# Optimization experiments

Measured on AMD Instinct MI355X. Metric: run time of the kernel, lower is better.

## Reference

```python
import jax, jax.numpy as jnp
import numpy as np

N = 100000       # nodes
E = 3200000      # edges (avg degree 32)
NFEAT = 500
NHID = 256
NCLASS = 40
NLAYERS = 5
EPS = 1e-5


def layer_norm(x, g, b):
    mu = jnp.mean(x, axis=-1, keepdims=True)
    var = jnp.mean(jnp.square(x - mu), axis=-1, keepdims=True)
    return (x - mu) * jax.lax.rsqrt(var + EPS) * g + b


def spmm(row, col, val, x):
    # out[i] = sum_{e: row[e]==i} val[e] * x[col[e]]  == adj @ x
    return jax.ops.segment_sum(val[:, None] * x[col], row, num_segments=N)


def setup_inputs() -> dict:
    key = jax.random.key(0)
    ks = jax.random.split(key, 10)
    s_in = 1.0 / np.sqrt(NFEAT)
    s_h = 1.0 / np.sqrt(NHID)
    return {
        "x": jax.random.normal(ks[0], (N, NFEAT), jnp.float32),
        "row": jax.random.randint(ks[1], (E,), 0, N, jnp.int32),
        "col": jax.random.randint(ks[2], (E,), 0, N, jnp.int32),
        "val": jax.random.uniform(ks[3], (E,), jnp.float32) * (1.0 / 32.0),
        "in_W": jax.random.normal(ks[4], (NHID, NFEAT), jnp.float32) * s_in,
        "in_b": jnp.zeros((NHID,), jnp.float32),
        "convW": jax.random.normal(ks[5], (NLAYERS, NHID, NHID), jnp.float32) * s_h,
        "convB": jnp.zeros((NLAYERS, NHID), jnp.float32),
        "lnG": jnp.ones((NLAYERS, NHID), jnp.float32),
        "lnB": jnp.zeros((NLAYERS, NHID), jnp.float32),
        "outG": jnp.ones((NHID,), jnp.float32),
        "outB": jnp.zeros((NHID,), jnp.float32),
        "out_W": jax.random.normal(ks[6], (NCLASS, NHID), jnp.float32) * s_h,
        "out_b": jnp.zeros((NCLASS,), jnp.float32),
        "only_z": 1,
    }


def reference(x, row, col, val, in_W, in_b, convW, convB, lnG, lnB,
              outG, outB, out_W, out_b, only_z):
    # input layer (input_dropout=0, so dropout is identity)
    h = jax.nn.relu(x @ in_W.T + in_b)
    # residual GCN layers with pre-LayerNorm (norm['flag'] == True)
    for i in range(NLAYERS):
        r = layer_norm(h, lnG[i], lnB[i])
        r = spmm(row, col, val, r)          # sparse aggregation
        r = r @ convW[i].T + convB[i]       # single linear (n_linear=1)
        if i < NLAYERS - 1:                 # last conv has last_layer=True -> no act
            r = jax.nn.relu(r)
        h = h + r
    mid = h                                 # captured at i == n_layers-1 (post-residual)
    z = layer_norm(h, outG, outB) @ out_W.T + out_b  # squeeze(1) is a no-op for nclass=40
    if only_z:
        return z
    return (mid, z)
```

## Files before the change

### kernel.cpp

```cpp
#include <hip/hip_runtime.h>
#include <stdint.h>

#define NFEAT 500
#define KPAD  512
#define NHID  256
#define NCLS  40
#define NCPAD 48
#define NLAY  5
#define BSH   8
#define CHUNK 8192

typedef __attribute__((ext_vector_type(8))) short short8;
typedef __attribute__((ext_vector_type(4))) float f32x4;

__device__ __forceinline__ ushort f2bf(float f) {
  uint32_t u = __float_as_uint(f);
  u += 0x7fffu + ((u >> 16) & 1u);
  return (ushort)(u >> 16);
}
__device__ __forceinline__ float b2f(ushort h) {
  return __uint_as_float(((uint32_t)h) << 16);
}

__global__ __launch_bounds__(256) void k_cast_pad(const float* __restrict__ src,
    ushort* __restrict__ dst, int rows, int scol, int dcol) {
  int id = blockIdx.x * 256 + threadIdx.x;
  int cpr = dcol >> 2;
  if (id >= rows * cpr) return;
  int r = id / cpr;
  int c = (id % cpr) * 4;
  float4 v;
  if (c + 3 < scol) {
    v = *(const float4*)(src + (size_t)r * scol + c);
  } else {
    v.x = (c + 0 < scol) ? src[(size_t)r * scol + c + 0] : 0.f;
    v.y = (c + 1 < scol) ? src[(size_t)r * scol + c + 1] : 0.f;
    v.z = (c + 2 < scol) ? src[(size_t)r * scol + c + 2] : 0.f;
    v.w = (c + 3 < scol) ? src[(size_t)r * scol + c + 3] : 0.f;
  }
  ushort4 o;
  o.x = f2bf(v.x); o.y = f2bf(v.y); o.z = f2bf(v.z); o.w = f2bf(v.w);
  *(ushort4*)(dst + (size_t)r * dcol + c) = o;
}

__global__ __launch_bounds__(256) void kA_scatter(const int* __restrict__ row,
    const int* __restrict__ col, const float* __restrict__ val,
    int* __restrict__ ccur, int2* __restrict__ pb, int E, int P, int CAP) {
  __shared__ int lh[512];
  const int t = threadIdx.x;
  const int b0 = blockIdx.x * CHUNK;
  for (int i = t; i < P; i += 256) lh[i] = 0;
  __syncthreads();
#pragma unroll 4
  for (int i = 0; i < CHUNK / 256; i++) {
    int idx = b0 + i * 256 + t;
    if (idx < E) atomicAdd(&lh[row[idx] >> BSH], 1);
  }
  __syncthreads();
  for (int i = t; i < P; i += 256) {
    int c = lh[i];
    lh[i] = (c > 0) ? atomicAdd(&ccur[i], c) : 0;
  }
  __syncthreads();
#pragma unroll 4
  for (int i = 0; i < CHUNK / 256; i++) {
    int idx = b0 + i * 256 + t;
    if (idx < E) {
      int r = row[idx];
      int p = r >> BSH;
      int pos = atomicAdd(&lh[p], 1);
      if (pos < CAP)
        pb[(size_t)p * CAP + pos] =
            make_int2(col[idx] | ((r & 255) << 24), __float_as_int(val[idx]));
    }
  }
}

__global__ __launch_bounds__(256) void kB_cnt(const int* __restrict__ ccur,
    const int2* __restrict__ pb, int* __restrict__ cnt, int* __restrict__ bsum,
    int N, int CAP) {
  __shared__ int lc[256];
  __shared__ int ws[4];
  const int b = blockIdx.x;
  const int t = threadIdx.x;
  lc[t] = 0;
  __syncthreads();
  int cb = min(ccur[b], CAP);
  size_t base = (size_t)b * CAP;
  for (int i = t; i < cb; i += 256)
    atomicAdd(&lc[((uint32_t)pb[base + i].x) >> 24], 1);
  __syncthreads();
  int c = lc[t];
  int r = (b << BSH) + t;
  if (r < N) cnt[r] = c;
  int v = c;
  v += __shfl_xor(v, 1); v += __shfl_xor(v, 2); v += __shfl_xor(v, 4);
  v += __shfl_xor(v, 8); v += __shfl_xor(v, 16); v += __shfl_xor(v, 32);
  if ((t & 63) == 0) ws[t >> 6] = v;
  __syncthreads();
  if (t == 0) bsum[b] = ws[0] + ws[1] + ws[2] + ws[3];
}

__global__ __launch_bounds__(1024) void k_scanP(const int* __restrict__ bsum,
    int* __restrict__ boff, int* __restrict__ ptrN, int P) {
  __shared__ int ls[1024];
  int t = threadIdx.x;
  int v = (t < P) ? bsum[t] : 0;
  ls[t] = v;
  __syncthreads();
  for (int off = 1; off < 1024; off <<= 1) {
    int u = (t >= off) ? ls[t - off] : 0;
    __syncthreads();
    ls[t] += u;
    __syncthreads();
  }
  if (t < P) boff[t] = ls[t] - v;
  if (t == 1023) *ptrN = ls[1023];
}

__global__ __launch_bounds__(256) void kB_ptr(const int* __restrict__ cnt,
    const int* __restrict__ boff, int* __restrict__ ptr, int N) {
  __shared__ int ls[256];
  int b = blockIdx.x;
  int t = threadIdx.x;
  int r = (b << BSH) + t;
  int v = (r < N) ? cnt[r] : 0;
  ls[t] = v;
  __syncthreads();
  for (int off = 1; off < 256; off <<= 1) {
    int u = (t >= off) ? ls[t - off] : 0;
    __syncthreads();
    ls[t] += u;
    __syncthreads();
  }
  if (r < N) ptr[r] = boff[b] + ls[t] - v;
}

__global__ __launch_bounds__(256) void kB_scatter(const int* __restrict__ ccur,
    const int2* __restrict__ pb, const int* __restrict__ ptr,
    int2* __restrict__ cv, int CAP) {
  __shared__ int rk[256];
  const int b = blockIdx.x;
  rk[threadIdx.x] = 0;
  __syncthreads();
  int cb = min(ccur[b], CAP);
  size_t base = (size_t)b * CAP;
  for (int i = threadIdx.x; i < cb; i += 256) {
    int2 p2 = pb[base + i];
    int r8 = ((uint32_t)p2.x) >> 24;
    int r = (b << BSH) + r8;
    int rank = atomicAdd(&rk[r8], 1);
    cv[ptr[r] + rank] = make_int2(p2.x & 0x00FFFFFF, p2.y);
  }
}

template<int FP8OUT>
__global__ __launch_bounds__(256) void k_ln(const float* __restrict__ h,
    const float* __restrict__ g, const float* __restrict__ b,
    void* __restrict__ o, int n) {
  int r = (blockIdx.x * 256 + threadIdx.x) >> 6;
  int lane = threadIdx.x & 63;
  if (r >= n) return;
  float4 v = *(const float4*)(h + (size_t)r * NHID + lane * 4);
  float s = v.x + v.y + v.z + v.w;
  s += __shfl_xor(s, 1); s += __shfl_xor(s, 2); s += __shfl_xor(s, 4);
  s += __shfl_xor(s, 8); s += __shfl_xor(s, 16); s += __shfl_xor(s, 32);
  float mu = s * (1.f / NHID);
  float d0 = v.x - mu, d1 = v.y - mu, d2 = v.z - mu, d3 = v.w - mu;
  float q = d0 * d0 + d1 * d1 + d2 * d2 + d3 * d3;
  q += __shfl_xor(q, 1); q += __shfl_xor(q, 2); q += __shfl_xor(q, 4);
  q += __shfl_xor(q, 8); q += __shfl_xor(q, 16); q += __shfl_xor(q, 32);
  float rs = rsqrtf(q * (1.f / NHID) + 1e-5f);
  float4 gv = *(const float4*)(g + lane * 4);
  float4 bv = *(const float4*)(b + lane * 4);
  float o0 = d0 * rs * gv.x + bv.x;
  float o1 = d1 * rs * gv.y + bv.y;
  float o2 = d2 * rs * gv.z + bv.z;
  float o3 = d3 * rs * gv.w + bv.w;
  if (FP8OUT) {
    int w = 0;
    w = __builtin_amdgcn_cvt_pk_fp8_f32(o0, o1, w, false);
    w = __builtin_amdgcn_cvt_pk_fp8_f32(o2, o3, w, true);
    ((uint32_t*)o)[(size_t)r * 64 + lane] = (uint32_t)w;
  } else {
    ushort4 t;
    t.x = f2bf(o0); t.y = f2bf(o1); t.z = f2bf(o2); t.w = f2bf(o3);
    *(ushort4*)((ushort*)o + (size_t)r * NHID + lane * 4) = t;
  }
}

__global__ __launch_bounds__(256) void k_spmm(const int* __restrict__ ptr,
    const int2* __restrict__ cv, const uint32_t* __restrict__ t8,
    ushort* __restrict__ agg, int n) {
  int r = (blockIdx.x * 256 + threadIdx.x) >> 6;
  int lane = threadIdx.x & 63;
  if (r >= n) return;
  int s = ptr[r], e = ptr[r + 1];
  int cnt = e - s;
  int half = lane >> 5;
  int seg = lane & 31;
  float acc[8];
#pragma unroll
  for (int j = 0; j < 8; j++) acc[j] = 0.f;

  for (int base = 0; base < cnt; base += 64) {
    int idx = s + base + lane;
    int ec = 0; float ev = 0.f;
    if (idx < e) {
      int2 p2 = cv[idx];
      ec = p2.x;
      ev = __uint_as_float((uint32_t)p2.y);
    }
    int lim = min(64, cnt - base);
#pragma unroll 2
    for (int i = 0; i < lim; i += 2) {
      int a = i + half;
      int c = __shfl(ec, a);
      float v = __shfl(ev, a);
      uint2 tv = *(const uint2*)(t8 + (size_t)c * 64 + seg * 2);
      auto p0 = __builtin_amdgcn_cvt_pk_f32_fp8(tv.x, false);
      auto p1 = __builtin_amdgcn_cvt_pk_f32_fp8(tv.x, true);
      auto p2 = __builtin_amdgcn_cvt_pk_f32_fp8(tv.y, false);
      auto p3 = __builtin_amdgcn_cvt_pk_f32_fp8(tv.y, true);
      acc[0] += v * p0[0]; acc[1] += v * p0[1];
      acc[2] += v * p1[0]; acc[3] += v * p1[1];
      acc[4] += v * p2[0]; acc[5] += v * p2[1];
      acc[6] += v * p3[0]; acc[7] += v * p3[1];
    }
  }

#pragma unroll
  for (int j = 0; j < 8; j++) acc[j] += __shfl_xor(acc[j], 32);
  if (half == 0) {
    short8 o;
#pragma unroll
    for (int j = 0; j < 8; j++) o[j] = (short)f2bf(acc[j]);
    *(short8*)(agg + (size_t)r * NHID + seg * 8) = o;
  }
}

template<int MODE>
__global__ __launch_bounds__(256) void k_gemm(const ushort* __restrict__ A,
    const ushort* __restrict__ B, const float* __restrict__ bias,
    float* __restrict__ H, int M, int K) {
  __shared__ ushort As[128 * 32];
  __shared__ ushort Bs[128 * 32];
  const int t = threadIdx.x;
  const int lane = t & 63;
  const int wid = t >> 6;
  const int brow = blockIdx.x * 128;
  const int bcol = blockIdx.y * 128;
  const int wr = (wid >> 1) * 64;
  const int wc = (wid & 1) * 64;
  const int l15 = lane & 15, hi = lane >> 4;
  const f32x4 z4 = {0.f, 0.f, 0.f, 0.f};
  f32x4 acc[4][4];
  for (int m = 0; m < 4; m++)
    for (int n = 0; n < 4; n++) acc[m][n] = z4;

  for (int k0 = 0; k0 < K; k0 += 32) {
    __syncthreads();
#pragma unroll
    for (int c = 0; c < 2; c++) {
      int s = c * 256 + t;
      int r = s >> 2;
      int kk = (s & 3) * 8;
      int gr = brow + r; gr = gr < M ? gr : M - 1;
      const ushort* ga = A + (size_t)gr * K + (k0 + kk);
      __builtin_amdgcn_global_load_lds((const __attribute__((address_space(1))) void*)ga,
          (__attribute__((address_space(3))) void*)(As + s * 8), 16, 0, 0);
      const ushort* gb = B + (size_t)(bcol + r) * K + (k0 + kk);
      __builtin_amdgcn_global_load_lds((const __attribute__((address_space(1))) void*)gb,
          (__attribute__((address_space(3))) void*)(Bs + s * 8), 16, 0, 0);
    }
    __syncthreads();
    short8 af[4], bf[4];
#pragma unroll
    for (int m = 0; m < 4; m++)
      af[m] = *(const short8*)(As + (wr + m * 16 + l15) * 32 + hi * 8);
#pragma unroll
    for (int n = 0; n < 4; n++)
      bf[n] = *(const short8*)(Bs + (wc + n * 16 + l15) * 32 + hi * 8);
#pragma unroll
    for (int m = 0; m < 4; m++)
#pragma unroll
      for (int n = 0; n < 4; n++)
        acc[m][n] = __builtin_amdgcn_mfma_f32_16x16x32_bf16(af[m], bf[n], acc[m][n], 0, 0, 0);
  }

#pragma unroll
  for (int m = 0; m < 4; m++) {
    int gr0 = brow + wr + m * 16 + hi * 4;
#pragma unroll
    for (int n = 0; n < 4; n++) {
      int gc = bcol + wc + n * 16 + l15;
      float bv = bias[gc];
#pragma unroll
      for (int j = 0; j < 4; j++) {
        int gr = gr0 + j;
        if (gr < M) {
          size_t idx = (size_t)gr * NHID + gc;
          float v = acc[m][n][j] + bv;
          if (MODE == 0)      H[idx] = fmaxf(v, 0.f);
          else if (MODE == 1) H[idx] += fmaxf(v, 0.f);
          else                H[idx] += v;
        }
      }
    }
  }
}

__global__ __launch_bounds__(256) void k_ogemm(const ushort* __restrict__ A,
    const ushort* __restrict__ Bw, const float* __restrict__ ob,
    float* __restrict__ z, int M) {
  __shared__ ushort As[256 * 32];
  __shared__ ushort Bs[NCPAD * 264];
  const int t = threadIdx.x;
  const int lane = t & 63;
  const int wid = t >> 6;
  const int brow = blockIdx.x * 256;
  const int wr = wid * 64;
  const int l15 = lane & 15, hi = lane >> 4;
  const f32x4 z4 = {0.f, 0.f, 0.f, 0.f};
  f32x4 acc[4][3];
#pragma unroll
  for (int m = 0; m < 4; m++)
#pragma unroll
    for (int n = 0; n < 3; n++) acc[m][n] = z4;

  for (int i = t; i < NCPAD * 33; i += 256) {
    int r = i / 33, cc = i % 33;
    if (cc < 32)
      *(short8*)(Bs + r * 264 + cc * 8) = *(const short8*)(Bw + r * 256 + cc * 8);
  }

  for (int k0 = 0; k0 < 256; k0 += 32) {
    __syncthreads();
#pragma unroll
    for (int c = 0; c < 4; c++) {
      int s = c * 256 + t;
      int r = s >> 2;
      int kk = (s & 3) * 8;
      int gr = brow + r; gr = gr < M ? gr : M - 1;
      const ushort* ga = A + (size_t)gr * NHID + (k0 + kk);
      __builtin_amdgcn_global_load_lds((const __attribute__((address_space(1))) void*)ga,
          (__attribute__((address_space(3))) void*)(As + s * 8), 16, 0, 0);
    }
    __syncthreads();
    short8 af[4], bf[3];
#pragma unroll
    for (int m = 0; m < 4; m++)
      af[m] = *(const short8*)(As + (wr + m * 16 + l15) * 32 + hi * 8);
#pragma unroll
    for (int n = 0; n < 3; n++)
      bf[n] = *(const short8*)(Bs + (n * 16 + l15) * 264 + k0 + hi * 8);
#pragma unroll
    for (int m = 0; m < 4; m++)
#pragma unroll
      for (int n = 0; n < 3; n++)
        acc[m][n] = __builtin_amdgcn_mfma_f32_16x16x32_bf16(af[m], bf[n], acc[m][n], 0, 0, 0);
  }

#pragma unroll
  for (int m = 0; m < 4; m++) {
    int gr0 = brow + wr + m * 16 + hi * 4;
#pragma unroll
    for (int n = 0; n < 3; n++) {
      int gc = n * 16 + l15;
      if (gc < NCLS) {
        float bv = ob[gc];
#pragma unroll
        for (int j = 0; j < 4; j++) {
          int gr = gr0 + j;
          if (gr < M) z[(size_t)gr * NCLS + gc] = acc[m][n][j] + bv;
        }
      }
    }
  }
}

extern "C" void kernel_launch(void* const* d_in, const int* in_sizes, int n_in,
                              void* d_out, int out_size, void* d_ws, size_t ws_size,
                              hipStream_t stream) {
  const float* x     = (const float*)d_in[0];
  const int*   row   = (const int*)d_in[1];
  const int*   col   = (const int*)d_in[2];
  const float* val   = (const float*)d_in[3];
  const float* inW   = (const float*)d_in[4];
  const float* inB   = (const float*)d_in[5];
  const float* convW = (const float*)d_in[6];
  const float* convB = (const float*)d_in[7];
  const float* lnG   = (const float*)d_in[8];
  const float* lnB   = (const float*)d_in[9];
  const float* outG  = (const float*)d_in[10];
  const float* outB  = (const float*)d_in[11];
  const float* outW  = (const float*)d_in[12];
  const float* outb  = (const float*)d_in[13];
  const int N = in_sizes[0] / NFEAT;
  const int E = in_sizes[1];
  float* z = (float*)d_out;

  const int P   = (N + 255) >> BSH;
  const int CAP = ((((E + P - 1) / P) * 5 / 4 + 256) + 15) & ~15;

  char* wsp = (char*)d_ws;
  size_t off = 0;
  auto alloc = [&](size_t bytes) {
    void* p = wsp + off;
    off += (bytes + 255) & ~(size_t)255;
    return p;
  };
  float*    h   = (float*)alloc((size_t)N * NHID * 4);
  ushort*   tb  = (ushort*)alloc((size_t)N * NHID * 2);
  ushort*   ab  = (ushort*)alloc((size_t)N * NHID * 2);
  uint32_t* t8  = (uint32_t*)alloc((size_t)N * 64 * 4);
  ushort*   xb  = (ushort*)alloc((size_t)N * KPAD * 2);
  ushort*   wbi = (ushort*)alloc((size_t)NHID * KPAD * 2);
  ushort*   wbc = (ushort*)alloc((size_t)NLAY * NHID * NHID * 2);
  ushort*   wbo = (ushort*)alloc((size_t)NCPAD * NHID * 2);
  int*   cnt  = (int*)alloc((size_t)N * 4);
  int*   ptr  = (int*)alloc((size_t)(N + 1) * 4);
  int*   ccur = (int*)alloc((size_t)P * 4);
  int*   bsum = (int*)alloc((size_t)P * 4);
  int*   boff = (int*)alloc((size_t)P * 4);
  int2*  cv   = (int2*)alloc((size_t)E * 8);
  int2*  pb   = (int2*)xb;

  {
    int tot = N * (KPAD >> 2);
    k_cast_pad<<<(tot + 255) / 256, 256, 0, stream>>>(x, xb, N, NFEAT, KPAD);
    tot = NHID * (KPAD >> 2);
    k_cast_pad<<<(tot + 255) / 256, 256, 0, stream>>>(inW, wbi, NHID, NFEAT, KPAD);
    tot = NLAY * NHID * (NHID >> 2);
    k_cast_pad<<<(tot + 255) / 256, 256, 0, stream>>>(convW, wbc, NLAY * NHID, NHID, NHID);
    hipMemsetAsync(wbo, 0, (size_t)NCPAD * NHID * 2, stream);
    tot = NCLS * (NHID >> 2);
    k_cast_pad<<<(tot + 255) / 256, 256, 0, stream>>>(outW, wbo, NCLS, NHID, NHID);
  }

  dim3 gg((N + 127) / 128, NHID / 128);
  k_gemm<0><<<gg, 256, 0, stream>>>(xb, wbi, inB, h, N, KPAD);

  hipMemsetAsync(ccur, 0, (size_t)P * 4, stream);
  kA_scatter<<<(E + CHUNK - 1) / CHUNK, 256, 0, stream>>>(row, col, val, ccur, pb, E, P, CAP);
  kB_cnt<<<P, 256, 0, stream>>>(ccur, pb, cnt, bsum, N, CAP);
  k_scanP<<<1, 1024, 0, stream>>>(bsum, boff, ptr + N, P);
  kB_ptr<<<P, 256, 0, stream>>>(cnt, boff, ptr, N);
  kB_scatter<<<P, 256, 0, stream>>>(ccur, pb, ptr, cv, CAP);

  int nwb = (N + 3) / 4;
  for (int i = 0; i < NLAY; i++) {
    k_ln<1><<<nwb, 256, 0, stream>>>(h, lnG + i * NHID, lnB + i * NHID, t8, N);
    k_spmm<<<nwb, 256, 0, stream>>>(ptr, cv, t8, ab, N);
    if (i < NLAY - 1)
      k_gemm<1><<<gg, 256, 0, stream>>>(ab, wbc + (size_t)i * NHID * NHID,
                                        convB + i * NHID, h, N, NHID);
    else
      k_gemm<2><<<gg, 256, 0, stream>>>(ab, wbc + (size_t)i * NHID * NHID,
                                        convB + i * NHID, h, N, NHID);
  }

  k_ln<0><<<nwb, 256, 0, stream>>>(h, outG, outB, tb, N);
  k_ogemm<<<(N + 255) / 256, 256, 0, stream>>>(tb, wbo, outb, z, N);
}
```

Measured before the change: 1.421 ms.

## Store residual hidden state in bf16 and widen SpMM per-lane gathers

The residual stream h changes from fp32 to bf16, which halves the read-modify-write traffic in the GEMM epilogues and the reads in the LayerNorm kernels. Separately, the SpMM kernel now has each lane load 16 fp8 values (uint4) and processes four edges per wave iteration instead of two, then reduces across quarter-waves. Accumulating the residual in bf16 through five layers lowers precision. The SpMM change also raises register use per thread and leaves fewer lanes writing output.

```diff
diff --git a/kernel.cpp b/kernel.cpp
--- a/kernel.cpp
+++ b/kernel.cpp
@@ -155,18 +155,19 @@
 }
 
 template<int FP8OUT>
-__global__ __launch_bounds__(256) void k_ln(const float* __restrict__ h,
+__global__ __launch_bounds__(256) void k_ln(const ushort* __restrict__ h,
     const float* __restrict__ g, const float* __restrict__ b,
     void* __restrict__ o, int n) {
   int r = (blockIdx.x * 256 + threadIdx.x) >> 6;
   int lane = threadIdx.x & 63;
   if (r >= n) return;
-  float4 v = *(const float4*)(h + (size_t)r * NHID + lane * 4);
-  float s = v.x + v.y + v.z + v.w;
+  ushort4 hv = *(const ushort4*)(h + (size_t)r * NHID + lane * 4);
+  float v0 = b2f(hv.x), v1 = b2f(hv.y), v2 = b2f(hv.z), v3 = b2f(hv.w);
+  float s = v0 + v1 + v2 + v3;
   s += __shfl_xor(s, 1); s += __shfl_xor(s, 2); s += __shfl_xor(s, 4);
   s += __shfl_xor(s, 8); s += __shfl_xor(s, 16); s += __shfl_xor(s, 32);
   float mu = s * (1.f / NHID);
-  float d0 = v.x - mu, d1 = v.y - mu, d2 = v.z - mu, d3 = v.w - mu;
+  float d0 = v0 - mu, d1 = v1 - mu, d2 = v2 - mu, d3 = v3 - mu;
   float q = d0 * d0 + d1 * d1 + d2 * d2 + d3 * d3;
   q += __shfl_xor(q, 1); q += __shfl_xor(q, 2); q += __shfl_xor(q, 4);
   q += __shfl_xor(q, 8); q += __shfl_xor(q, 16); q += __shfl_xor(q, 32);
@@ -197,11 +198,11 @@
   if (r >= n) return;
   int s = ptr[r], e = ptr[r + 1];
   int cnt = e - s;
-  int half = lane >> 5;
-  int seg = lane & 31;
-  float acc[8];
-#pragma unroll
-  for (int j = 0; j < 8; j++) acc[j] = 0.f;
+  int q = lane >> 4;
+  int seg = lane & 15;
+  float acc[16];
+#pragma unroll
+  for (int j = 0; j < 16; j++) acc[j] = 0.f;
 
   for (int base = 0; base < cnt; base += 64) {
     int idx = s + base + lane;
@@ -213,36 +214,48 @@
     }
     int lim = min(64, cnt - base);
 #pragma unroll 2
-    for (int i = 0; i < lim; i += 2) {
-      int a = i + half;
+    for (int i = 0; i < lim; i += 4) {
+      int a = i + q;
       int c = __shfl(ec, a);
       float v = __shfl(ev, a);
-      uint2 tv = *(const uint2*)(t8 + (size_t)c * 64 + seg * 2);
+      uint4 tv = *(const uint4*)(t8 + (size_t)c * 64 + seg * 4);
       auto p0 = __builtin_amdgcn_cvt_pk_f32_fp8(tv.x, false);
       auto p1 = __builtin_amdgcn_cvt_pk_f32_fp8(tv.x, true);
       auto p2 = __builtin_amdgcn_cvt_pk_f32_fp8(tv.y, false);
       auto p3 = __builtin_amdgcn_cvt_pk_f32_fp8(tv.y, true);
-      acc[0] += v * p0[0]; acc[1] += v * p0[1];
-      acc[2] += v * p1[0]; acc[3] += v * p1[1];
-      acc[4] += v * p2[0]; acc[5] += v * p2[1];
-      acc[6] += v * p3[0]; acc[7] += v * p3[1];
-    }
-  }
-
-#pragma unroll
-  for (int j = 0; j < 8; j++) acc[j] += __shfl_xor(acc[j], 32);
-  if (half == 0) {
-    short8 o;
-#pragma unroll
-    for (int j = 0; j < 8; j++) o[j] = (short)f2bf(acc[j]);
-    *(short8*)(agg + (size_t)r * NHID + seg * 8) = o;
+      auto p4 = __builtin_amdgcn_cvt_pk_f32_fp8(tv.z, false);
+      auto p5 = __builtin_amdgcn_cvt_pk_f32_fp8(tv.z, true);
+      auto p6 = __builtin_amdgcn_cvt_pk_f32_fp8(tv.w, false);
+      auto p7 = __builtin_amdgcn_cvt_pk_f32_fp8(tv.w, true);
+      acc[0]  += v * p0[0]; acc[1]  += v * p0[1];
+      acc[2]  += v * p1[0]; acc[3]  += v * p1[1];
+      acc[4]  += v * p2[0]; acc[5]  += v * p2[1];
+      acc[6]  += v * p3[0]; acc[7]  += v * p3[1];
+      acc[8]  += v * p4[0]; acc[9]  += v * p4[1];
+      acc[10] += v * p5[0]; acc[11] += v * p5[1];
+      acc[12] += v * p6[0]; acc[13] += v * p6[1];
+      acc[14] += v * p7[0]; acc[15] += v * p7[1];
+    }
+  }
+
+#pragma unroll
+  for (int j = 0; j < 16; j++) {
+    acc[j] += __shfl_xor(acc[j], 16);
+    acc[j] += __shfl_xor(acc[j], 32);
+  }
+  if (q == 0) {
+    short8 o0, o1;
+#pragma unroll
+    for (int j = 0; j < 8; j++) { o0[j] = (short)f2bf(acc[j]); o1[j] = (short)f2bf(acc[8 + j]); }
+    *(short8*)(agg + (size_t)r * NHID + seg * 16) = o0;
+    *(short8*)(agg + (size_t)r * NHID + seg * 16 + 8) = o1;
   }
 }
 
 template<int MODE>
 __global__ __launch_bounds__(256) void k_gemm(const ushort* __restrict__ A,
     const ushort* __restrict__ B, const float* __restrict__ bias,
-    float* __restrict__ H, int M, int K) {
+    ushort* __restrict__ H, int M, int K) {
   __shared__ ushort As[128 * 32];
   __shared__ ushort Bs[128 * 32];
   const int t = threadIdx.x;
@@ -301,9 +314,9 @@
         if (gr < M) {
           size_t idx = (size_t)gr * NHID + gc;
           float v = acc[m][n][j] + bv;
-          if (MODE == 0)      H[idx] = fmaxf(v, 0.f);
-          else if (MODE == 1) H[idx] += fmaxf(v, 0.f);
-          else                H[idx] += v;
+          if (MODE == 0)      H[idx] = f2bf(fmaxf(v, 0.f));
+          else if (MODE == 1) H[idx] = f2bf(b2f(H[idx]) + fmaxf(v, 0.f));
+          else                H[idx] = f2bf(b2f(H[idx]) + v);
         }
       }
     }
@@ -410,7 +423,7 @@
     off += (bytes + 255) & ~(size_t)255;
     return p;
   };
-  float*    h   = (float*)alloc((size_t)N * NHID * 4);
+  ushort*   h   = (ushort*)alloc((size_t)N * NHID * 2);
   ushort*   tb  = (ushort*)alloc((size_t)N * NHID * 2);
   ushort*   ab  = (ushort*)alloc((size_t)N * NHID * 2);
   uint32_t* t8  = (uint32_t*)alloc((size_t)N * 64 * 4);
```

Result: faster. 1.259 ms (-11.4%).
